# Performance work log

Measured on AMD Instinct MI355X. Metric: run time of the kernel, lower is better.

## Reference

```python
import jax, jax.numpy as jnp
import numpy as np

NUM_GRAPHS = 256
NEG_SLOPE = 0.2


def gat_layer(x, src, dst, W, a_src, a_dst, bias, concat):
    # x: [N, Fin], W: [Fin, H*C], a_src/a_dst: [H, C], bias: [H*C] or [C]
    N = x.shape[0]
    H, C = a_src.shape
    xl = (x @ W).reshape(N, H, C)                      # per-head projections
    e_src = jnp.sum(xl * a_src, axis=-1)               # [N, H]
    e_dst = jnp.sum(xl * a_dst, axis=-1)               # [N, H]
    e = jax.nn.leaky_relu(e_src[src] + e_dst[dst], NEG_SLOPE)  # [E, H]
    # edge softmax over variable-size neighbor sets (grouped by dst)
    m = jax.ops.segment_max(e, dst, num_segments=N)    # [N, H]
    m = jnp.where(jnp.isfinite(m), m, 0.0)
    ee = jnp.exp(e - m[dst])
    s = jax.ops.segment_sum(ee, dst, num_segments=N)   # [N, H]
    alpha = ee / (s[dst] + 1e-16)                      # [E, H]
    msg = alpha[:, :, None] * xl[src]                  # [E, H, C]
    out = jax.ops.segment_sum(msg, dst, num_segments=N)  # [N, H, C]
    out = out.reshape(N, H * C) if concat else out.mean(axis=1)
    return out + bias


def setup_inputs() -> dict:
    key = jax.random.key(0)
    ks = jax.random.split(key, 12)
    N, E, Fin, H, C, Fout = 100000, 1600000, 128, 8, 16, 64
    x = jax.random.normal(ks[0], (N, Fin), dtype=jnp.float32)
    edge_index = jax.random.randint(ks[1], (2, E), 0, N, dtype=jnp.int32)
    batch = jnp.sort(jax.random.randint(ks[2], (N,), 0, NUM_GRAPHS, dtype=jnp.int32))
    sc = 0.1
    W1 = jax.random.normal(ks[3], (Fin, H * C), dtype=jnp.float32) * sc
    att_src1 = jax.random.normal(ks[4], (H, C), dtype=jnp.float32) * sc
    att_dst1 = jax.random.normal(ks[5], (H, C), dtype=jnp.float32) * sc
    bias1 = jnp.zeros((H * C,), dtype=jnp.float32)
    W2 = jax.random.normal(ks[6], (H * C, Fout), dtype=jnp.float32) * sc
    att_src2 = jax.random.normal(ks[7], (1, Fout), dtype=jnp.float32) * sc
    att_dst2 = jax.random.normal(ks[8], (1, Fout), dtype=jnp.float32) * sc
    bias2 = jnp.zeros((Fout,), dtype=jnp.float32)
    return {"x": x, "W1": W1, "att_src1": att_src1, "att_dst1": att_dst1,
            "bias1": bias1, "W2": W2, "att_src2": att_src2, "att_dst2": att_dst2,
            "bias2": bias2, "edge_index": edge_index, "batch": batch}


def reference(x, W1, att_src1, att_dst1, bias1, W2, att_src2, att_dst2, bias2,
              edge_index, batch):
    N = x.shape[0]
    loop = jnp.arange(N, dtype=edge_index.dtype)
    src = jnp.concatenate([edge_index[0], loop])  # add self-loops (PyG default)
    dst = jnp.concatenate([edge_index[1], loop])
    # dropout is identity in eval mode
    h = gat_layer(x, src, dst, W1, att_src1, att_dst1, bias1, concat=True)
    h = jax.nn.elu(h)
    h = gat_layer(h, src, dst, W2, att_src2, att_dst2, bias2, concat=False)
    # global mean pooling over graphs
    sums = jax.ops.segment_sum(h, batch, num_segments=NUM_GRAPHS)
    cnts = jax.ops.segment_sum(jnp.ones((N,), h.dtype), batch, num_segments=NUM_GRAPHS)
    return sums / jnp.maximum(cnts, 1.0)[:, None]
```

## Files before the change

kernel.cpp:

```cpp
#include <hip/hip_runtime.h>
#include <hip/hip_fp16.h>


#define LRELU_SLOPE 0.2f
#define NBLKB 512
#define NBUCK 256

__device__ __forceinline__ float lrelu(float x) { return x > 0.f ? x : LRELU_SLOPE * x; }

typedef _Float16 f16x8 __attribute__((ext_vector_type(8)));
typedef float f32x4 __attribute__((ext_vector_type(4)));

__global__ __launch_bounds__(256) void convWT2(const float* __restrict__ W1,
    const float* __restrict__ W2, __half* __restrict__ Wt1, __half* __restrict__ Wt2) {
  const int i = blockIdx.x * 256 + threadIdx.x;
  if (i < 128 * 128) {
    const int k = i >> 7, m = i & 127;
    Wt1[m * 128 + k] = __float2half(W1[i]);
  } else {
    const int j = i - 128 * 128;
    if (j < 128 * 64) {
      const int k = j >> 6, m = j & 63;
      Wt2[m * 128 + k] = __float2half(W2[j]);
    }
  }
}

template<typename TX, int M_, int HEADS>
__global__ __launch_bounds__(256) void gemm_mfma(const TX* __restrict__ X,
    const __half* __restrict__ Wt, __half* __restrict__ Y,
    const float* __restrict__ as, const float* __restrict__ ad,
    float* __restrict__ es, float* __restrict__ ed, int N) {
  constexpr int K = 128;
  constexpr int BM = 64;
  constexpr int LP = K + 8;
  __shared__ _Float16 Xl[BM * LP];
  const int tid = threadIdx.x;
  const int row0 = blockIdx.x * BM;

  if constexpr (sizeof(TX) == 4) {
    for (int i = tid; i < BM * (K / 4); i += 256) {
      const int r = i / (K / 4), c4 = (i % (K / 4)) * 4;
      int gr = row0 + r; if (gr >= N) gr = N - 1;
      const float4 v = *(const float4*)((const float*)X + (size_t)gr * K + c4);
      _Float16* d = &Xl[r * LP + c4];
      d[0] = (_Float16)v.x; d[1] = (_Float16)v.y;
      d[2] = (_Float16)v.z; d[3] = (_Float16)v.w;
    }
  } else {
    for (int i = tid; i < BM * (K / 8); i += 256) {
      const int r = i / (K / 8), c8 = (i % (K / 8)) * 8;
      int gr = row0 + r; if (gr >= N) gr = N - 1;
      const f16x8 v = *(const f16x8*)((const _Float16*)X + (size_t)gr * K + c8);
      *(f16x8*)&Xl[r * LP + c8] = v;
    }
  }
  __syncthreads();

  const int w = tid >> 6, l = tid & 63;
  const int lrow = l & 15, lk = (l >> 4) * 8;
  constexpr int NT = M_ / 16;
  f32x4 acc[NT];
#pragma unroll
  for (int n = 0; n < NT; ++n) acc[n] = (f32x4){0.f, 0.f, 0.f, 0.f};

#pragma unroll
  for (int kk = 0; kk < K; kk += 32) {
    const f16x8 a = *(const f16x8*)&Xl[(w * 16 + lrow) * LP + kk + lk];
#pragma unroll
    for (int n = 0; n < NT; ++n) {
      const f16x8 b = *(const f16x8*)((const _Float16*)Wt +
                        (size_t)(n * 16 + lrow) * K + kk + lk);
      acc[n] = __builtin_amdgcn_mfma_f32_16x16x32_f16(a, b, acc[n], 0, 0, 0);
    }
  }
  const int orow = row0 + w * 16 + (l >> 4) * 4;
#pragma unroll
  for (int n = 0; n < NT; ++n) {
#pragma unroll
    for (int j = 0; j < 4; ++j) {
      const int gr = orow + j;
      if (gr < N) Y[(size_t)gr * M_ + n * 16 + lrow] = __float2half(acc[n][j]);
    }
  }

  if constexpr (HEADS == 8) {
#pragma unroll
    for (int n = 0; n < NT; ++n) {
#pragma unroll
      for (int j = 0; j < 4; ++j) {
        float ps = acc[n][j] * as[n * 16 + lrow];
        float pd = acc[n][j] * ad[n * 16 + lrow];
#pragma unroll
        for (int o = 1; o <= 8; o <<= 1) {
          ps += __shfl_xor(ps, o);
          pd += __shfl_xor(pd, o);
        }
        if (lrow == n) {
          const int gr = orow + j;
          if (gr < N) { es[gr * 8 + n] = ps; ed[gr * 8 + n] = pd; }
        }
      }
    }
  } else {
#pragma unroll
    for (int j = 0; j < 4; ++j) {
      float ps = 0.f, pd = 0.f;
#pragma unroll
      for (int n = 0; n < NT; ++n) {
        ps += acc[n][j] * as[n * 16 + lrow];
        pd += acc[n][j] * ad[n * 16 + lrow];
      }
#pragma unroll
      for (int o = 1; o <= 8; o <<= 1) {
        ps += __shfl_xor(ps, o);
        pd += __shfl_xor(pd, o);
      }
      if (lrow == 0) {
        const int gr = orow + j;
        if (gr < N) { es[gr] = ps; ed[gr] = pd; }
      }
    }
  }
}

__global__ __launch_bounds__(1024) void bucket_hist(const int* __restrict__ ei, int E,
    int* __restrict__ bh) {
  __shared__ int hist[NBUCK];
  const int t = threadIdx.x;
  if (t < NBUCK) hist[t] = 0;
  __syncthreads();
  const int chunk = (E + NBLKB - 1) / NBLKB;
  const int s0 = blockIdx.x * chunk;
  const int s1 = min(E, s0 + chunk);
  for (int e = s0 + t; e < s1; e += 1024) atomicAdd(&hist[ei[E + e] >> 9], 1);
  __syncthreads();
  if (t < NBUCK) bh[t * NBLKB + blockIdx.x] = hist[t];
}

__global__ __launch_bounds__(256) void scanA(int* __restrict__ a, int* __restrict__ ctot, int N) {
  __shared__ int sm[256];
  const int base = blockIdx.x * 1024;
  const int t = threadIdx.x;
  int v[4], s = 0;
#pragma unroll
  for (int i = 0; i < 4; ++i) {
    const int idx = base + t * 4 + i;
    v[i] = (idx < N) ? a[idx] : 0;
    s += v[i];
  }
  sm[t] = s;
  __syncthreads();
  for (int o = 1; o < 256; o <<= 1) {
    const int x = (t >= o) ? sm[t - o] : 0;
    __syncthreads();
    sm[t] += x;
    __syncthreads();
  }
  if (t == 255) ctot[blockIdx.x] = sm[255];
  int run = sm[t] - s;
#pragma unroll
  for (int i = 0; i < 4; ++i) {
    const int idx = base + t * 4 + i;
    if (idx < N) a[idx] = run;
    run += v[i];
  }
}

__global__ __launch_bounds__(128) void scanB(int* __restrict__ ctot, int n) {
  __shared__ int sm[128];
  const int t = threadIdx.x;
  const int v = (t < n) ? ctot[t] : 0;
  sm[t] = v;
  __syncthreads();
  for (int o = 1; o < 128; o <<= 1) {
    const int x = (t >= o) ? sm[t - o] : 0;
    __syncthreads();
    sm[t] += x;
    __syncthreads();
  }
  if (t < n) ctot[t] = sm[t] - v;
}

__global__ __launch_bounds__(256) void scanC(int* __restrict__ a, const int* __restrict__ ctot, int N) {
  const int i = blockIdx.x * 256 + threadIdx.x;
  if (i < N) a[i] += ctot[i >> 10];
}

__global__ __launch_bounds__(1024) void bucket_scatter(const int* __restrict__ ei, int E,
    const int* __restrict__ bh, int* __restrict__ eb) {
  __shared__ int offs[NBUCK];
  const int t = threadIdx.x;
  if (t < NBUCK) offs[t] = bh[t * NBLKB + blockIdx.x];
  __syncthreads();
  const int chunk = (E + NBLKB - 1) / NBLKB;
  const int s0 = blockIdx.x * chunk;
  const int s1 = min(E, s0 + chunk);
  for (int e = s0 + t; e < s1; e += 1024) {
    const int s = ei[e], d = ei[E + e];
    const int pos = atomicAdd(&offs[d >> 9], 1);
    eb[pos] = (s << 9) | (d & 511);
  }
}

__global__ __launch_bounds__(512) void csr_bucket(const int* __restrict__ eb,
    const int* __restrict__ bh, int E, int N,
    int* __restrict__ rowptr, int* __restrict__ csr) {
  __shared__ int deg[512];
  __shared__ int sm[512];
  const int t = threadIdx.x;
  const int bucket = blockIdx.x;
  const int bstart = bh[bucket * NBLKB];
  const int bend = (bucket + 1 < NBUCK) ? bh[(bucket + 1) * NBLKB] : E;
  const int n0 = bucket << 9;
  deg[t] = 0;
  __syncthreads();
  for (int j = bstart + t; j < bend; j += 512) atomicAdd(&deg[eb[j] & 511], 1);
  __syncthreads();
  const int v = deg[t];
  sm[t] = v;
  __syncthreads();
  for (int o = 1; o < 512; o <<= 1) {
    const int x = (t >= o) ? sm[t - o] : 0;
    __syncthreads();
    sm[t] += x;
    __syncthreads();
  }
  if (n0 + t < N) rowptr[n0 + t] = bstart + sm[t];
  deg[t] = bstart + sm[t] - v;
  __syncthreads();
  for (int j = bstart + t; j < bend; j += 512) {
    const int e = eb[j];
    const int pos = atomicAdd(&deg[e & 511], 1);
    csr[pos] = e >> 9;
  }
}

__global__ __launch_bounds__(256) void gather_h8(const __half* __restrict__ xl,
    const float* __restrict__ es, const float* __restrict__ ed,
    const int* __restrict__ rowptr, const int* __restrict__ csr,
    const float* __restrict__ bias, __half* __restrict__ hout, int N) {
  const int wave = threadIdx.x >> 6, lane = threadIdx.x & 63;
  const int n = blockIdx.x * 4 + wave;
  if (n >= N) return;
  const int sub = lane >> 5;
  const int sl  = lane & 31;
  const int c0  = sl * 4;
  const int h   = sl >> 2;
  const float edv = ed[n * 8 + h];
  const int start = (n == 0) ? 0 : rowptr[n - 1];
  const int end   = rowptr[n];
  union U8 { uint2 u; __half2 h2[2]; };

  float4 acc = make_float4(0.f, 0.f, 0.f, 0.f);
  float ssum = 0.f;
  if (sub == 0) {
    const float ee = __expf(lrelu(es[n * 8 + h] + edv));
    U8 r; r.u = *(const uint2*)&xl[(size_t)n * 128 + c0];
    const float2 f0 = __half22float2(r.h2[0]), f1 = __half22float2(r.h2[1]);
    acc.x = ee * f0.x; acc.y = ee * f0.y; acc.z = ee * f1.x; acc.w = ee * f1.y;
    ssum = ee;
  }
  int j = start + sub;
  for (; j + 6 < end; j += 8) {
    int s0 = csr[j], s1 = csr[j + 2], s2 = csr[j + 4], s3 = csr[j + 6];
    float ev[4]; U8 r[4];
    ev[0] = es[s0 * 8 + h]; r[0].u = *(const uint2*)&xl[(size_t)s0 * 128 + c0];
    ev[1] = es[s1 * 8 + h]; r[1].u = *(const uint2*)&xl[(size_t)s1 * 128 + c0];
    ev[2] = es[s2 * 8 + h]; r[2].u = *(const uint2*)&xl[(size_t)s2 * 128 + c0];
    ev[3] = es[s3 * 8 + h]; r[3].u = *(const uint2*)&xl[(size_t)s3 * 128 + c0];
#pragma unroll
    for (int k = 0; k < 4; ++k) {
      const float ee = __expf(lrelu(ev[k] + edv));
      const float2 f0 = __half22float2(r[k].h2[0]), f1 = __half22float2(r[k].h2[1]);
      acc.x += ee * f0.x; acc.y += ee * f0.y;
      acc.z += ee * f1.x; acc.w += ee * f1.y;
      ssum += ee;
    }
  }
  for (; j < end; j += 2) {
    const int src = csr[j];
    const float ee = __expf(lrelu(es[src * 8 + h] + edv));
    U8 r; r.u = *(const uint2*)&xl[(size_t)src * 128 + c0];
    const float2 f0 = __half22float2(r.h2[0]), f1 = __half22float2(r.h2[1]);
    acc.x += ee * f0.x; acc.y += ee * f0.y;
    acc.z += ee * f1.x; acc.w += ee * f1.y;
    ssum += ee;
  }
  acc.x += __shfl_xor(acc.x, 32); acc.y += __shfl_xor(acc.y, 32);
  acc.z += __shfl_xor(acc.z, 32); acc.w += __shfl_xor(acc.w, 32);
  ssum  += __shfl_xor(ssum, 32);
  if (sub == 0) {
    const float inv = 1.f / (ssum + 1e-16f);
    const float4 b4 = *(const float4*)&bias[c0];
    float v0 = acc.x * inv + b4.x, v1 = acc.y * inv + b4.y;
    float v2 = acc.z * inv + b4.z, v3 = acc.w * inv + b4.w;
    v0 = v0 > 0.f ? v0 : __expf(v0) - 1.f;
    v1 = v1 > 0.f ? v1 : __expf(v1) - 1.f;
    v2 = v2 > 0.f ? v2 : __expf(v2) - 1.f;
    v3 = v3 > 0.f ? v3 : __expf(v3) - 1.f;
    U8 o; o.h2[0] = __floats2half2_rn(v0, v1); o.h2[1] = __floats2half2_rn(v2, v3);
    *(uint2*)&hout[(size_t)n * 128 + c0] = o.u;
  }
}

__global__ __launch_bounds__(256) void gather_h1(const __half* __restrict__ xl2,
    const float* __restrict__ es, const float* __restrict__ ed,
    const int* __restrict__ rowptr, const int* __restrict__ csr,
    const float* __restrict__ bias, float* __restrict__ vout, int N) {
  const int wave = threadIdx.x >> 6, lane = threadIdx.x & 63;
  const int n = blockIdx.x * 4 + wave;
  if (n >= N) return;
  const int sub = lane >> 4;
  const int sl  = lane & 15;
  const int c0  = sl * 4;
  const float edv = ed[n];
  const int start = (n == 0) ? 0 : rowptr[n - 1];
  const int end   = rowptr[n];
  union U8 { uint2 u; __half2 h2[2]; };

  float4 acc = make_float4(0.f, 0.f, 0.f, 0.f);
  float ssum = 0.f;
  if (sub == 0) {
    const float ee = __expf(lrelu(es[n] + edv));
    U8 r; r.u = *(const uint2*)&xl2[(size_t)n * 64 + c0];
    const float2 f0 = __half22float2(r.h2[0]), f1 = __half22float2(r.h2[1]);
    acc.x = ee * f0.x; acc.y = ee * f0.y; acc.z = ee * f1.x; acc.w = ee * f1.y;
    ssum = ee;
  }
  int j = start + sub;
  for (; j + 4 < end; j += 8) {
    const int s0 = csr[j], s1 = csr[j + 4];
    const float e0 = es[s0], e1 = es[s1];
    U8 r0, r1;
    r0.u = *(const uint2*)&xl2[(size_t)s0 * 64 + c0];
    r1.u = *(const uint2*)&xl2[(size_t)s1 * 64 + c0];
    {
      const float ee = __expf(lrelu(e0 + edv));
      const float2 f0 = __half22float2(r0.h2[0]), f1 = __half22float2(r0.h2[1]);
      acc.x += ee * f0.x; acc.y += ee * f0.y;
      acc.z += ee * f1.x; acc.w += ee * f1.y; ssum += ee;
    }
    {
      const float ee = __expf(lrelu(e1 + edv));
      const float2 f0 = __half22float2(r1.h2[0]), f1 = __half22float2(r1.h2[1]);
      acc.x += ee * f0.x; acc.y += ee * f0.y;
      acc.z += ee * f1.x; acc.w += ee * f1.y; ssum += ee;
    }
  }
  for (; j < end; j += 4) {
    const int src = csr[j];
    const float ee = __expf(lrelu(es[src] + edv));
    U8 r; r.u = *(const uint2*)&xl2[(size_t)src * 64 + c0];
    const float2 f0 = __half22float2(r.h2[0]), f1 = __half22float2(r.h2[1]);
    acc.x += ee * f0.x; acc.y += ee * f0.y;
    acc.z += ee * f1.x; acc.w += ee * f1.y; ssum += ee;
  }
#pragma unroll
  for (int o = 16; o <= 32; o <<= 1) {
    acc.x += __shfl_xor(acc.x, o); acc.y += __shfl_xor(acc.y, o);
    acc.z += __shfl_xor(acc.z, o); acc.w += __shfl_xor(acc.w, o);
    ssum  += __shfl_xor(ssum, o);
  }
  if (sub == 0) {
    const float inv = 1.f / (ssum + 1e-16f);
    const float4 b4 = *(const float4*)&bias[c0];
    float4 o;
    o.x = acc.x * inv + b4.x; o.y = acc.y * inv + b4.y;
    o.z = acc.z * inv + b4.z; o.w = acc.w * inv + b4.w;
    *(float4*)&vout[(size_t)n * 64 + c0] = o;
  }
}

__global__ __launch_bounds__(256) void pool_seg(const float* __restrict__ v,
    const int* __restrict__ batch, float* __restrict__ out, int N) {
  const int g = blockIdx.x;
  const int t = threadIdx.x;
  int lo = 0, hi = N;
  while (lo < hi) { const int m = (lo + hi) >> 1; if (batch[m] < g) lo = m + 1; else hi = m; }
  const int start = lo;
  hi = N;
  while (lo < hi) { const int m = (lo + hi) >> 1; if (batch[m] <= g) lo = m + 1; else hi = m; }
  const int end = lo;

  const int c = t & 63, rg = t >> 6;
  float s = 0.f;
  for (int r = start + rg; r < end; r += 4) s += v[(size_t)r * 64 + c];
  __shared__ float sm[256];
  sm[t] = s;
  __syncthreads();
  if (t < 64) {
    const float tot = sm[t] + sm[t + 64] + sm[t + 128] + sm[t + 192];
    out[g * 64 + t] = tot / fmaxf((float)(end - start), 1.f);
  }
}

extern "C" void kernel_launch(void* const* d_in, const int* in_sizes, int n_in,
                              void* d_out, int out_size, void* d_ws, size_t ws_size,
                              hipStream_t stream) {
  const float* x   = (const float*)d_in[0];
  const float* W1  = (const float*)d_in[1];
  const float* as1 = (const float*)d_in[2];
  const float* ad1 = (const float*)d_in[3];
  const float* b1  = (const float*)d_in[4];
  const float* W2  = (const float*)d_in[5];
  const float* as2 = (const float*)d_in[6];
  const float* ad2 = (const float*)d_in[7];
  const float* b2  = (const float*)d_in[8];
  const int* ei    = (const int*)d_in[9];
  const int* batch = (const int*)d_in[10];
  float* out = (float*)d_out;
  const int N = in_sizes[10];
  const int E = in_sizes[9] / 2;
  const int G = out_size / 64;
  const int BH = NBUCK * NBLKB;

  char* ws = (char*)d_ws;
  __half* xl  = (__half*)ws;
  __half* h   = (__half*)(ws + (size_t)N * 256);
  __half* xl2 = xl;
  float* vbuf = (float*)(ws + (size_t)N * 256);
  float* es1  = (float*)(ws + (size_t)N * 512);
  float* ed1  = es1 + (size_t)N * 8;
  float* es2  = es1;
  float* ed2  = es1 + N;
  int* rowptr = (int*)(ed1 + (size_t)N * 8);
  int* csr    = rowptr + N;
  int* eb     = csr + E;
  int* bh     = eb + E;
  int* ctot   = bh + BH;
  __half* Wt1 = (__half*)((((uintptr_t)(ctot + 128)) + 31) & ~(uintptr_t)31);
  __half* Wt2 = Wt1 + 128 * 128;

  convWT2<<<(128 * 128 + 128 * 64 + 255) / 256, 256, 0, stream>>>(W1, W2, Wt1, Wt2);

  bucket_hist<<<NBLKB, 1024, 0, stream>>>(ei, E, bh);
  scanA<<<BH / 1024, 256, 0, stream>>>(bh, ctot, BH);
  scanB<<<1, 128, 0, stream>>>(ctot, BH / 1024);
  scanC<<<BH / 256, 256, 0, stream>>>(bh, ctot, BH);
  bucket_scatter<<<NBLKB, 1024, 0, stream>>>(ei, E, bh, eb);
  csr_bucket<<<(N + 511) / 512, 512, 0, stream>>>(eb, bh, E, N, rowptr, csr);

  gemm_mfma<float, 128, 8><<<(N + 63) / 64, 256, 0, stream>>>(x, Wt1, xl, as1, ad1, es1, ed1, N);
  gather_h8<<<(N + 3) / 4, 256, 0, stream>>>(xl, es1, ed1, rowptr, csr, b1, h, N);

  gemm_mfma<__half, 64, 1><<<(N + 63) / 64, 256, 0, stream>>>(h, Wt2, xl2, as2, ad2, es2, ed2, N);
  gather_h1<<<(N + 3) / 4, 256, 0, stream>>>(xl2, es2, ed2, rowptr, csr, b2, vbuf, N);

  pool_seg<<<G, 256, 0, stream>>>(vbuf, batch, out, N);
}
```

Measured before the change: 286.9 us.

## Fuse setup kernels, sort CSR by source band, use exp2 with prescaled logits

Merges the weight conversion kernel into the histogram kernel, and folds the small ctot scan into scanC so each block rescans the 128 chunk totals, removing two launches. It prescales the attention logits by log2(e) in the GEMM epilogue so the gather kernels can call exp2f instead of __expf. The CSR build now scatters edges in passes over source bands of 8192 nodes, so neighbours within each row are roughly grouped by source, which should improve cache locality for the later gathers. The banded scatter rereads each bucket's edge list once per band, about 13 times, which adds work to csr_bucket.

```diff
diff --git a/kernel.cpp b/kernel.cpp
--- a/kernel.cpp
+++ b/kernel.cpp
@@ -5,26 +5,12 @@
 #define LRELU_SLOPE 0.2f
 #define NBLKB 512
 #define NBUCK 256
+#define LOG2E 1.4426950408889634f
 
 __device__ __forceinline__ float lrelu(float x) { return x > 0.f ? x : LRELU_SLOPE * x; }
 
 typedef _Float16 f16x8 __attribute__((ext_vector_type(8)));
 typedef float f32x4 __attribute__((ext_vector_type(4)));
-
-__global__ __launch_bounds__(256) void convWT2(const float* __restrict__ W1,
-    const float* __restrict__ W2, __half* __restrict__ Wt1, __half* __restrict__ Wt2) {
-  const int i = blockIdx.x * 256 + threadIdx.x;
-  if (i < 128 * 128) {
-    const int k = i >> 7, m = i & 127;
-    Wt1[m * 128 + k] = __float2half(W1[i]);
-  } else {
-    const int j = i - 128 * 128;
-    if (j < 128 * 64) {
-      const int k = j >> 6, m = j & 63;
-      Wt2[m * 128 + k] = __float2half(W2[j]);
-    }
-  }
-}
 
 template<typename TX, int M_, int HEADS>
 __global__ __launch_bounds__(256) void gemm_mfma(const TX* __restrict__ X,
@@ -98,7 +84,7 @@
         }
         if (lrow == n) {
           const int gr = orow + j;
-          if (gr < N) { es[gr * 8 + n] = ps; ed[gr * 8 + n] = pd; }
+          if (gr < N) { es[gr * 8 + n] = ps * LOG2E; ed[gr * 8 + n] = pd * LOG2E; }
         }
       }
     }
@@ -118,24 +104,37 @@
       }
       if (lrow == 0) {
         const int gr = orow + j;
-        if (gr < N) { es[gr] = ps; ed[gr] = pd; }
+        if (gr < N) { es[gr] = ps * LOG2E; ed[gr] = pd * LOG2E; }
       }
     }
   }
 }
 
-__global__ __launch_bounds__(1024) void bucket_hist(const int* __restrict__ ei, int E,
-    int* __restrict__ bh) {
-  __shared__ int hist[NBUCK];
-  const int t = threadIdx.x;
-  if (t < NBUCK) hist[t] = 0;
-  __syncthreads();
-  const int chunk = (E + NBLKB - 1) / NBLKB;
-  const int s0 = blockIdx.x * chunk;
-  const int s1 = min(E, s0 + chunk);
-  for (int e = s0 + t; e < s1; e += 1024) atomicAdd(&hist[ei[E + e] >> 9], 1);
-  __syncthreads();
-  if (t < NBUCK) bh[t * NBLKB + blockIdx.x] = hist[t];
+__global__ __launch_bounds__(1024) void hist_conv(const int* __restrict__ ei, int E,
+    int* __restrict__ bh, const float* __restrict__ W1, const float* __restrict__ W2,
+    __half* __restrict__ Wt1, __half* __restrict__ Wt2) {
+  const int t = threadIdx.x;
+  if (blockIdx.x < NBLKB) {
+    __shared__ int hist[NBUCK];
+    if (t < NBUCK) hist[t] = 0;
+    __syncthreads();
+    const int chunk = (E + NBLKB - 1) / NBLKB;
+    const int s0 = blockIdx.x * chunk;
+    const int s1 = min(E, s0 + chunk);
+    for (int e = s0 + t; e < s1; e += 1024) atomicAdd(&hist[ei[E + e] >> 9], 1);
+    __syncthreads();
+    if (t < NBUCK) bh[t * NBLKB + blockIdx.x] = hist[t];
+  } else {
+    const int i = (blockIdx.x - NBLKB) * 1024 + t;
+    if (i < 128 * 128) {
+      const int k = i >> 7, m = i & 127;
+      Wt1[m * 128 + k] = __float2half(W1[i]);
+    } else if (i < 128 * 128 + 128 * 64) {
+      const int j = i - 128 * 128;
+      const int k = j >> 6, m = j & 63;
+      Wt2[m * 128 + k] = __float2half(W2[j]);
+    }
+  }
 }
 
 __global__ __launch_bounds__(256) void scanA(int* __restrict__ a, int* __restrict__ ctot, int N) {
@@ -167,24 +166,24 @@
   }
 }
 
-__global__ __launch_bounds__(128) void scanB(int* __restrict__ ctot, int n) {
-  __shared__ int sm[128];
-  const int t = threadIdx.x;
-  const int v = (t < n) ? ctot[t] : 0;
-  sm[t] = v;
+__global__ __launch_bounds__(256) void scanC(int* __restrict__ a,
+    const int* __restrict__ ctot, int NCH, int Ntot) {
+  __shared__ int sc[128];
+  const int t = threadIdx.x;
+  if (t < 128) sc[t] = (t < NCH) ? ctot[t] : 0;
   __syncthreads();
   for (int o = 1; o < 128; o <<= 1) {
-    const int x = (t >= o) ? sm[t - o] : 0;
-    __syncthreads();
-    sm[t] += x;
-    __syncthreads();
-  }
-  if (t < n) ctot[t] = sm[t] - v;
-}
-
-__global__ __launch_bounds__(256) void scanC(int* __restrict__ a, const int* __restrict__ ctot, int N) {
-  const int i = blockIdx.x * 256 + threadIdx.x;
-  if (i < N) a[i] += ctot[i >> 10];
+    int x = 0;
+    if (t < 128 && t >= o) x = sc[t - o];
+    __syncthreads();
+    if (t < 128) sc[t] += x;
+    __syncthreads();
+  }
+  const int i = blockIdx.x * 256 + t;
+  if (i < Ntot) {
+    const int c = i >> 10;
+    a[i] += (c == 0) ? 0 : sc[c - 1];
+  }
 }
 
 __global__ __launch_bounds__(1024) void bucket_scatter(const int* __restrict__ ei, int E,
@@ -229,10 +228,15 @@
   if (n0 + t < N) rowptr[n0 + t] = bstart + sm[t];
   deg[t] = bstart + sm[t] - v;
   __syncthreads();
-  for (int j = bstart + t; j < bend; j += 512) {
-    const int e = eb[j];
-    const int pos = atomicAdd(&deg[e & 511], 1);
-    csr[pos] = e >> 9;
+  const int nband = (N + 8191) >> 13;
+  for (int b = 0; b < nband; ++b) {
+    for (int j = bstart + t; j < bend; j += 512) {
+      const int e = eb[j];
+      if ((e >> 22) == b) {
+        const int pos = atomicAdd(&deg[e & 511], 1);
+        csr[pos] = e >> 9;
+      }
+    }
   }
 }
 
@@ -255,7 +259,7 @@
   float4 acc = make_float4(0.f, 0.f, 0.f, 0.f);
   float ssum = 0.f;
   if (sub == 0) {
-    const float ee = __expf(lrelu(es[n * 8 + h] + edv));
+    const float ee = exp2f(lrelu(es[n * 8 + h] + edv));
     U8 r; r.u = *(const uint2*)&xl[(size_t)n * 128 + c0];
     const float2 f0 = __half22float2(r.h2[0]), f1 = __half22float2(r.h2[1]);
     acc.x = ee * f0.x; acc.y = ee * f0.y; acc.z = ee * f1.x; acc.w = ee * f1.y;
@@ -271,7 +275,7 @@
     ev[3] = es[s3 * 8 + h]; r[3].u = *(const uint2*)&xl[(size_t)s3 * 128 + c0];
 #pragma unroll
     for (int k = 0; k < 4; ++k) {
-      const float ee = __expf(lrelu(ev[k] + edv));
+      const float ee = exp2f(lrelu(ev[k] + edv));
       const float2 f0 = __half22float2(r[k].h2[0]), f1 = __half22float2(r[k].h2[1]);
       acc.x += ee * f0.x; acc.y += ee * f0.y;
       acc.z += ee * f1.x; acc.w += ee * f1.y;
@@ -280,7 +284,7 @@
   }
   for (; j < end; j += 2) {
     const int src = csr[j];
-    const float ee = __expf(lrelu(es[src * 8 + h] + edv));
+    const float ee = exp2f(lrelu(es[src * 8 + h] + edv));
     U8 r; r.u = *(const uint2*)&xl[(size_t)src * 128 + c0];
     const float2 f0 = __half22float2(r.h2[0]), f1 = __half22float2(r.h2[1]);
     acc.x += ee * f0.x; acc.y += ee * f0.y;
@@ -322,7 +326,7 @@
   float4 acc = make_float4(0.f, 0.f, 0.f, 0.f);
   float ssum = 0.f;
   if (sub == 0) {
-    const float ee = __expf(lrelu(es[n] + edv));
+    const float ee = exp2f(lrelu(es[n] + edv));
     U8 r; r.u = *(const uint2*)&xl2[(size_t)n * 64 + c0];
     const float2 f0 = __half22float2(r.h2[0]), f1 = __half22float2(r.h2[1]);
     acc.x = ee * f0.x; acc.y = ee * f0.y; acc.z = ee * f1.x; acc.w = ee * f1.y;
@@ -336,13 +340,13 @@
     r0.u = *(const uint2*)&xl2[(size_t)s0 * 64 + c0];
     r1.u = *(const uint2*)&xl2[(size_t)s1 * 64 + c0];
     {
-      const float ee = __expf(lrelu(e0 + edv));
+      const float ee = exp2f(lrelu(e0 + edv));
       const float2 f0 = __half22float2(r0.h2[0]), f1 = __half22float2(r0.h2[1]);
       acc.x += ee * f0.x; acc.y += ee * f0.y;
       acc.z += ee * f1.x; acc.w += ee * f1.y; ssum += ee;
     }
     {
-      const float ee = __expf(lrelu(e1 + edv));
+      const float ee = exp2f(lrelu(e1 + edv));
       const float2 f0 = __half22float2(r1.h2[0]), f1 = __half22float2(r1.h2[1]);
       acc.x += ee * f0.x; acc.y += ee * f0.y;
       acc.z += ee * f1.x; acc.w += ee * f1.y; ssum += ee;
@@ -350,7 +354,7 @@
   }
   for (; j < end; j += 4) {
     const int src = csr[j];
-    const float ee = __expf(lrelu(es[src] + edv));
+    const float ee = exp2f(lrelu(es[src] + edv));
     U8 r; r.u = *(const uint2*)&xl2[(size_t)src * 64 + c0];
     const float2 f0 = __half22float2(r.h2[0]), f1 = __half22float2(r.h2[1]);
     acc.x += ee * f0.x; acc.y += ee * f0.y;
@@ -432,12 +436,9 @@
   __half* Wt1 = (__half*)((((uintptr_t)(ctot + 128)) + 31) & ~(uintptr_t)31);
   __half* Wt2 = Wt1 + 128 * 128;
 
-  convWT2<<<(128 * 128 + 128 * 64 + 255) / 256, 256, 0, stream>>>(W1, W2, Wt1, Wt2);
-
-  bucket_hist<<<NBLKB, 1024, 0, stream>>>(ei, E, bh);
+  hist_conv<<<NBLKB + 24, 1024, 0, stream>>>(ei, E, bh, W1, W2, Wt1, Wt2);
   scanA<<<BH / 1024, 256, 0, stream>>>(bh, ctot, BH);
-  scanB<<<1, 128, 0, stream>>>(ctot, BH / 1024);
-  scanC<<<BH / 256, 256, 0, stream>>>(bh, ctot, BH);
+  scanC<<<BH / 256, 256, 0, stream>>>(bh, ctot, BH / 1024, BH);
   bucket_scatter<<<NBLKB, 1024, 0, stream>>>(ei, E, bh, eb);
   csr_bucket<<<(N + 511) / 512, 512, 0, stream>>>(eb, bh, E, N, rowptr, csr);
 
```

Result: slower. 320.3 us (+11.6%).
